# Kernel optimization log

Hardware: AMD Instinct MI355X
Metric: run time of the kernel (lower is better)

The kernel has to match this reference:

```python
import jax, jax.numpy as jnp
import numpy as np

K_SIZE = 5      # kernel_size
NUM_ITERS = 3   # num_iters
EPS = 1e-6


def _unfold(x, k):
    """Mimic F.unfold(x, k, padding=k//2) -> (B, N, K, D) with K=k*k, N=H*W.
    Channel ordering matches torch: unfold gives (B, D*K, N) with d-major, so
    view(B, D, K, N).permute(0, 3, 2, 1) == transpose below."""
    B, D, H, W = x.shape
    p = k // 2
    xp = jnp.pad(x, ((0, 0), (0, 0), (p, p), (p, p)))
    # stack k*k shifted views -> (B, D, K, H, W); loop is over the fixed 5x5 window
    patches = jnp.stack([xp[:, :, i:i + H, j:j + W]
                         for i in range(k) for j in range(k)], axis=2)
    return patches.reshape(B, D, k * k, H * W).transpose(0, 3, 2, 1)  # (B,N,K,D)


def setup_inputs() -> dict:
    key = jax.random.key(0)
    embeddings = jax.random.normal(key, (2, 32, 256, 256), dtype=jnp.float32)
    # init_bandwidth=1.0 -> log(exp(1)-1) so softplus(log_bandwidth)=1.0
    log_bandwidth = jnp.asarray(np.log(np.exp(1.0) - 1.0), dtype=jnp.float32)
    return {"embeddings": embeddings, "log_bandwidth": log_bandwidth}


def reference(embeddings, log_bandwidth):
    B, D, H, W = embeddings.shape
    N = H * W
    z = embeddings.reshape(B, D, N).transpose(0, 2, 1)  # (B, N, D)
    bandwidth = jax.nn.softplus(log_bandwidth)
    inv_2bw2 = 1.0 / (2.0 * bandwidth * bandwidth)
    # NOTE: original code unfolds `embeddings` (not z) every iter -> constant patches
    patches = _unfold(embeddings, K_SIZE)  # (B, N, K, D)
    for _ in range(NUM_ITERS):
        z_flat = jax.lax.stop_gradient(z)  # matches z.detach()
        diff = patches - z_flat[:, :, None, :]           # (B, N, K, D)
        dist2 = jnp.sum(diff * diff, axis=-1)            # (B, N, K)
        weights = jnp.exp(-dist2 * inv_2bw2)             # gaussian kernel
        numerator = jnp.einsum('bnk,bnkd->bnd', weights, patches)
        denom = jnp.sum(weights, axis=2, keepdims=True) + EPS
        z = numerator / denom
    # default flags: only shifted embeddings are returned
    return z.transpose(0, 2, 1).reshape(B, D, H, W)
```

## Files before the change

### kernel.cpp

```cpp
#include <hip/hip_runtime.h>
#include <math.h>


typedef _Float16 h2  __attribute__((ext_vector_type(2)));
typedef _Float16 h8  __attribute__((ext_vector_type(8)));
typedef unsigned int u4v __attribute__((ext_vector_type(4)));

constexpr int Dch  = 32;
constexpr int HH   = 256;
constexpr int WW   = 256;
constexpr int PADp = 2;
constexpr int BH   = 8;
constexpr int BW   = 16;
constexpr int TH   = BH + 2 * PADp;
constexpr int TWd  = BW + 2 * PADp;
constexpr int RSTR = 21;
constexpr int PSTR = TH * RSTR + 1;
constexpr int ITERS = 3;
constexpr int HWp  = HH * WW;
constexpr int NTHR = 512;

__device__ __forceinline__ float fdot2f(h2 a, h2 b, float c) {
    return __builtin_amdgcn_fdot2(a, b, c, false);
}

__device__ __forceinline__ float EXP2F(float x) {
#if __has_builtin(__builtin_amdgcn_exp2f)
    return __builtin_amdgcn_exp2f(x);
#else
    return __expf(x * 0.69314718055994531f);
#endif
}

__device__ __forceinline__ float qswap1(float x) {
    return __int_as_float(
        __builtin_amdgcn_mov_dpp(__float_as_int(x), 0xB1, 0xF, 0xF, true));
}
__device__ __forceinline__ float qswap2(float x) {
    return __int_as_float(
        __builtin_amdgcn_mov_dpp(__float_as_int(x), 0x4E, 0xF, 0xF, true));
}

__device__ __forceinline__ h2 as_h2(unsigned int x) {
    return __builtin_bit_cast(h2, x);
}

__global__ __launch_bounds__(NTHR, 4)
void meanshift_kernel(const float* __restrict__ E,
                      const float* __restrict__ lbw,
                      float* __restrict__ out)
{
    __shared__ u4v tile[4 * PSTR];

    const int bz  = blockIdx.z;
    const int oh  = blockIdx.y * BH - PADp;
    const int ow  = blockIdx.x * BW - PADp;
    const int tid = threadIdx.x;
    const int cq  = tid & 3;
    const int idx = tid >> 2;
    const int px  = idx & (BW - 1);
    const int py  = idx >> 4;

    const float bwv   = log1pf(__expf(lbw[0]));
    const float cc2   = 1.0f / (2.0f * bwv * bwv);
    const float negNC = -cc2 * 1.44269504f;

    const float* Eb = E + (size_t)bz * Dch * HWp;

    for (int job = tid; job < 4 * (TH * TWd); job += NTHR) {
        const int cc = job / (TH * TWd);
        const int p  = job - cc * (TH * TWd);
        const int tr = p / TWd;
        const int tc = p - tr * TWd;
        const int gh = oh + tr;
        const int gw = ow + tc;
        h8 v;
        if ((unsigned)gh < (unsigned)HH && (unsigned)gw < (unsigned)WW) {
            const float* p0 = Eb + (size_t)(8 * cc) * HWp + gh * WW + gw;
            #pragma unroll
            for (int k = 0; k < 8; ++k) v[k] = (_Float16)p0[k * HWp];
        } else {
            #pragma unroll
            for (int k = 0; k < 8; ++k) v[k] = (_Float16)0.f;
        }
        tile[cc * PSTR + tr * RSTR + tc] = __builtin_bit_cast(u4v, v);
    }
    __syncthreads();

    const u4v* __restrict__ tP = tile + cq * PSTR;

    const int rb0 = (py + 0) * RSTR + px;
    const int rb1 = (py + 1) * RSTR + px;
    const int rb2 = (py + 2) * RSTR + px;
    const int rb3 = (py + 3) * RSTR + px;
    const int rb4 = (py + 4) * RSTR + px;
    const u4v c00 = tP[rb0+0], c01 = tP[rb0+1], c02 = tP[rb0+2], c03 = tP[rb0+3], c04 = tP[rb0+4];
    const u4v c10 = tP[rb1+0], c11 = tP[rb1+1], c12 = tP[rb1+2], c13 = tP[rb1+3], c14 = tP[rb1+4];
    const u4v c20 = tP[rb2+0], c21 = tP[rb2+1], c22 = tP[rb2+2], c23 = tP[rb2+3], c24 = tP[rb2+4];
    const u4v c30 = tP[rb3+0], c31 = tP[rb3+1], c32 = tP[rb3+2], c33 = tP[rb3+3], c34 = tP[rb3+4];
    const u4v c40 = tP[rb4+0], c41 = tP[rb4+1], c42 = tP[rb4+2], c43 = tP[rb4+3], c44 = tP[rb4+4];

    h2 z0 = as_h2(c22[0]), z1 = as_h2(c22[1]);
    h2 z2 = as_h2(c22[2]), z3 = as_h2(c22[3]);

    float* Ob = out + (size_t)bz * Dch * HWp;
    const int off    = (oh + PADp + py) * WW + (ow + PADp + px);
    const int chbase = 8 * cq;

#define NBODY(Q) do {                                                         \
        const h2 p0 = as_h2(Q[0]), p1 = as_h2(Q[1]);                          \
        const h2 p2 = as_h2(Q[2]), p3 = as_h2(Q[3]);                          \
        const h2 e0 = p0 - z0, e1 = p1 - z1;                                  \
        const h2 e2 = p2 - z2, e3 = p3 - z3;                                  \
        float s0 = fdot2f(e0, e0, 0.f);                                       \
        float s1 = fdot2f(e1, e1, 0.f);                                       \
        s0 = fdot2f(e2, e2, s0);                                              \
        s1 = fdot2f(e3, e3, s1);                                              \
        const float dp = s0 + s1;                          \
        const float d2 = dp + qswap1(dp);                                     \
        const float dist = d2 + qswap2(d2);             \
        const float w = EXP2F(dist * negNC);                                  \
        den += w;                                                             \
        const _Float16 wh = (_Float16)w;                                      \
        const h2 w2v = {wh, wh};                                              \
        n0 += p0 * w2v; n1 += p1 * w2v;                                       \
        n2 += p2 * w2v; n3 += p3 * w2v;                                       \
    } while (0)

    #pragma unroll 1
    for (int it = 0; it < ITERS; ++it) {
        h2 n0 = {(_Float16)0.f, (_Float16)0.f};
        h2 n1 = n0, n2 = n0, n3 = n0;
        float den = 0.f;

        NBODY(c00); NBODY(c01); NBODY(c02); NBODY(c03); NBODY(c04);
        NBODY(c10); NBODY(c11); NBODY(c12); NBODY(c13); NBODY(c14);
        NBODY(c20); NBODY(c21); NBODY(c22); NBODY(c23); NBODY(c24);
        NBODY(c30); NBODY(c31); NBODY(c32); NBODY(c33); NBODY(c34);
        NBODY(c40); NBODY(c41); NBODY(c42); NBODY(c43); NBODY(c44);

        const float invf = 1.0f / (den + 1e-6f);
        if (it == ITERS - 1) {
#define WR(IDX, NV, EL) Ob[(size_t)(chbase + (IDX)) * HWp + off] = (float)NV[EL] * invf
            WR(0, n0, 0); WR(1, n0, 1); WR(2, n1, 0); WR(3, n1, 1);
            WR(4, n2, 0); WR(5, n2, 1); WR(6, n3, 0); WR(7, n3, 1);
#undef WR
        } else {
            const _Float16 ih = (_Float16)invf;
            const h2 iv = {ih, ih};
            z0 = n0 * iv; z1 = n1 * iv; z2 = n2 * iv; z3 = n3 * iv;
        }
    }
#undef NBODY
}

extern "C" void kernel_launch(void* const* d_in, const int* in_sizes, int n_in,
                              void* d_out, int out_size, void* d_ws, size_t ws_size,
                              hipStream_t stream) {
    const float* E   = (const float*)d_in[0];
    const float* lbw = (const float*)d_in[1];
    float* out       = (float*)d_out;

    const int B = in_sizes[0] / (Dch * HWp);
    dim3 grid(WW / BW, HH / BH, B);
    dim3 block(NTHR, 1, 1);
    hipLaunchKernelGGL(meanshift_kernel, grid, block, 0, stream, E, lbw, out);
}
```

Baseline: 38.85 us.

## Vectorize halo tile loads with float4 and prescale embeddings to fold bandwidth

Rewrites the shared-memory tile fill so each thread loads four adjacent pixels per channel with float4 global loads. This replaces scalar strided loads and the generic job loop, which should cut global load instructions. The tile is widened to 24 columns with a 4-aligned left edge. Embeddings are prescaled by sqrt(bandwidth constant) so the exp2 argument needs no multiply; the scale is undone at the final store. It also uses packed round-toward-zero fp16 conversions and lowers launch bounds occupancy from 4 to 2, which may affect register allocation and precision slightly.

After: 41.04 us. +5.6%, slower.

```diff
diff --git a/kernel.cpp b/kernel.cpp
--- a/kernel.cpp
+++ b/kernel.cpp
@@ -3,19 +3,17 @@
 
 
 typedef _Float16 h2  __attribute__((ext_vector_type(2)));
-typedef _Float16 h8  __attribute__((ext_vector_type(8)));
 typedef unsigned int u4v __attribute__((ext_vector_type(4)));
 
 constexpr int Dch  = 32;
 constexpr int HH   = 256;
 constexpr int WW   = 256;
-constexpr int PADp = 2;
 constexpr int BH   = 8;
 constexpr int BW   = 16;
-constexpr int TH   = BH + 2 * PADp;
-constexpr int TWd  = BW + 2 * PADp;
-constexpr int RSTR = 21;
-constexpr int PSTR = TH * RSTR + 1;
+constexpr int THs  = 12;
+constexpr int RSTR = 25;
+constexpr int PSTR = THs * RSTR + 1;
+constexpr int NJOB = 4 * THs * 6;
 constexpr int ITERS = 3;
 constexpr int HWp  = HH * WW;
 constexpr int NTHR = 512;
@@ -45,7 +43,19 @@
     return __builtin_bit_cast(h2, x);
 }
 
-__global__ __launch_bounds__(NTHR, 4)
+__device__ __forceinline__ h2 pk2(float a, float b) {
+#if __has_builtin(__builtin_amdgcn_cvt_pkrtz)
+    return __builtin_bit_cast(h2, __builtin_amdgcn_cvt_pkrtz(a, b));
+#else
+    h2 r; r[0] = (_Float16)a; r[1] = (_Float16)b; return r;
+#endif
+}
+
+__device__ __forceinline__ unsigned int pku(float a, float b) {
+    return __builtin_bit_cast(unsigned int, pk2(a, b));
+}
+
+__global__ __launch_bounds__(NTHR, 2)
 void meanshift_kernel(const float* __restrict__ E,
                       const float* __restrict__ lbw,
                       float* __restrict__ out)
@@ -53,47 +63,82 @@
     __shared__ u4v tile[4 * PSTR];
 
     const int bz  = blockIdx.z;
-    const int oh  = blockIdx.y * BH - PADp;
-    const int ow  = blockIdx.x * BW - PADp;
+    const int oh  = blockIdx.y * BH - 2;
+    const int owc = blockIdx.x * BW;
+    const int gw0 = owc - 4;
     const int tid = threadIdx.x;
     const int cq  = tid & 3;
     const int idx = tid >> 2;
     const int px  = idx & (BW - 1);
     const int py  = idx >> 4;
 
-    const float bwv   = log1pf(__expf(lbw[0]));
-    const float cc2   = 1.0f / (2.0f * bwv * bwv);
-    const float negNC = -cc2 * 1.44269504f;
+    const float bwv = log1pf(__expf(lbw[0]));
+    const float cc2 = 1.0f / (2.0f * bwv * bwv);
+    const float NCf = cc2 * 1.44269504f;
+    const float scl = __builtin_sqrtf(NCf);
+    const float isc = 1.0f / scl;
 
     const float* Eb = E + (size_t)bz * Dch * HWp;
 
-    for (int job = tid; job < 4 * (TH * TWd); job += NTHR) {
-        const int cc = job / (TH * TWd);
-        const int p  = job - cc * (TH * TWd);
-        const int tr = p / TWd;
-        const int tc = p - tr * TWd;
-        const int gh = oh + tr;
-        const int gw = ow + tc;
-        h8 v;
-        if ((unsigned)gh < (unsigned)HH && (unsigned)gw < (unsigned)WW) {
-            const float* p0 = Eb + (size_t)(8 * cc) * HWp + gh * WW + gw;
-            #pragma unroll
-            for (int k = 0; k < 8; ++k) v[k] = (_Float16)p0[k * HWp];
-        } else {
-            #pragma unroll
-            for (int k = 0; k < 8; ++k) v[k] = (_Float16)0.f;
+    if (tid < NJOB) {
+        const int cc  = tid / (THs * 6);
+        const int rem = tid - cc * (THs * 6);
+        const int row = rem / 6;
+        const int g   = rem - row * 6;
+        const int gh  = oh + row;
+        const int gwb = gw0 + 4 * g;
+
+        float4 F0 = {0.f,0.f,0.f,0.f}, F1 = F0, F2 = F0, F3 = F0;
+        float4 F4 = F0, F5 = F0, F6 = F0, F7 = F0;
+        if ((unsigned)gh < (unsigned)HH) {
+            const float* base = Eb + (size_t)(8 * cc) * HWp + gh * WW;
+            if (gwb >= 0 && gwb + 4 <= WW) {
+                F0 = *(const float4*)(base + 0 * (size_t)HWp + gwb);
+                F1 = *(const float4*)(base + 1 * (size_t)HWp + gwb);
+                F2 = *(const float4*)(base + 2 * (size_t)HWp + gwb);
+                F3 = *(const float4*)(base + 3 * (size_t)HWp + gwb);
+                F4 = *(const float4*)(base + 4 * (size_t)HWp + gwb);
+                F5 = *(const float4*)(base + 5 * (size_t)HWp + gwb);
+                F6 = *(const float4*)(base + 6 * (size_t)HWp + gwb);
+                F7 = *(const float4*)(base + 7 * (size_t)HWp + gwb);
+            } else {
+                const bool i0 = (unsigned)(gwb + 0) < (unsigned)WW;
+                const bool i1 = (unsigned)(gwb + 1) < (unsigned)WW;
+                const bool i2 = (unsigned)(gwb + 2) < (unsigned)WW;
+                const bool i3 = (unsigned)(gwb + 3) < (unsigned)WW;
+#define GE(K) F##K = make_float4( \
+                    i0 ? base[(K) * (size_t)HWp + gwb + 0] : 0.f, \
+                    i1 ? base[(K) * (size_t)HWp + gwb + 1] : 0.f, \
+                    i2 ? base[(K) * (size_t)HWp + gwb + 2] : 0.f, \
+                    i3 ? base[(K) * (size_t)HWp + gwb + 3] : 0.f)
+                GE(0); GE(1); GE(2); GE(3); GE(4); GE(5); GE(6); GE(7);
+#undef GE
+            }
         }
-        tile[cc * PSTR + tr * RSTR + tc] = __builtin_bit_cast(u4v, v);
+        const int wbase = cc * PSTR + row * RSTR + 4 * g;
+        u4v W;
+        W[0]=pku(F0.x*scl,F1.x*scl); W[1]=pku(F2.x*scl,F3.x*scl);
+        W[2]=pku(F4.x*scl,F5.x*scl); W[3]=pku(F6.x*scl,F7.x*scl);
+        tile[wbase + 0] = W;
+        W[0]=pku(F0.y*scl,F1.y*scl); W[1]=pku(F2.y*scl,F3.y*scl);
+        W[2]=pku(F4.y*scl,F5.y*scl); W[3]=pku(F6.y*scl,F7.y*scl);
+        tile[wbase + 1] = W;
+        W[0]=pku(F0.z*scl,F1.z*scl); W[1]=pku(F2.z*scl,F3.z*scl);
+        W[2]=pku(F4.z*scl,F5.z*scl); W[3]=pku(F6.z*scl,F7.z*scl);
+        tile[wbase + 2] = W;
+        W[0]=pku(F0.w*scl,F1.w*scl); W[1]=pku(F2.w*scl,F3.w*scl);
+        W[2]=pku(F4.w*scl,F5.w*scl); W[3]=pku(F6.w*scl,F7.w*scl);
+        tile[wbase + 3] = W;
     }
     __syncthreads();
 
     const u4v* __restrict__ tP = tile + cq * PSTR;
 
-    const int rb0 = (py + 0) * RSTR + px;
-    const int rb1 = (py + 1) * RSTR + px;
-    const int rb2 = (py + 2) * RSTR + px;
-    const int rb3 = (py + 3) * RSTR + px;
-    const int rb4 = (py + 4) * RSTR + px;
+    const int rb0 = (py + 0) * RSTR + (px + 2);
+    const int rb1 = rb0 + RSTR;
+    const int rb2 = rb1 + RSTR;
+    const int rb3 = rb2 + RSTR;
+    const int rb4 = rb3 + RSTR;
     const u4v c00 = tP[rb0+0], c01 = tP[rb0+1], c02 = tP[rb0+2], c03 = tP[rb0+3], c04 = tP[rb0+4];
     const u4v c10 = tP[rb1+0], c11 = tP[rb1+1], c12 = tP[rb1+2], c13 = tP[rb1+3], c14 = tP[rb1+4];
     const u4v c20 = tP[rb2+0], c21 = tP[rb2+1], c22 = tP[rb2+2], c23 = tP[rb2+3], c24 = tP[rb2+4];
@@ -104,7 +149,7 @@
     h2 z2 = as_h2(c22[2]), z3 = as_h2(c22[3]);
 
     float* Ob = out + (size_t)bz * Dch * HWp;
-    const int off    = (oh + PADp + py) * WW + (ow + PADp + px);
+    const int off    = (oh + 2 + py) * WW + (owc + px);
     const int chbase = 8 * cq;
 
 #define NBODY(Q) do {                                                         \
@@ -116,13 +161,12 @@
         float s1 = fdot2f(e1, e1, 0.f);                                       \
         s0 = fdot2f(e2, e2, s0);                                              \
         s1 = fdot2f(e3, e3, s1);                                              \
-        const float dp = s0 + s1;                          \
+        const float dp = s0 + s1;                       \
         const float d2 = dp + qswap1(dp);                                     \
-        const float dist = d2 + qswap2(d2);             \
-        const float w = EXP2F(dist * negNC);                                  \
+        const float d4 = d2 + qswap2(d2);                     \
+        const float w  = EXP2F(-d4);                \
         den += w;                                                             \
-        const _Float16 wh = (_Float16)w;                                      \
-        const h2 w2v = {wh, wh};                                              \
+        const h2 w2v = pk2(w, w);                                             \
         n0 += p0 * w2v; n1 += p1 * w2v;                                       \
         n2 += p2 * w2v; n3 += p3 * w2v;                                       \
     } while (0)
@@ -141,13 +185,13 @@
 
         const float invf = 1.0f / (den + 1e-6f);
         if (it == ITERS - 1) {
-#define WR(IDX, NV, EL) Ob[(size_t)(chbase + (IDX)) * HWp + off] = (float)NV[EL] * invf
+            const float fin = invf * isc;
+#define WR(IDX, NV, EL) Ob[(size_t)(chbase + (IDX)) * HWp + off] = (float)NV[EL] * fin
             WR(0, n0, 0); WR(1, n0, 1); WR(2, n1, 0); WR(3, n1, 1);
             WR(4, n2, 0); WR(5, n2, 1); WR(6, n3, 0); WR(7, n3, 1);
 #undef WR
         } else {
-            const _Float16 ih = (_Float16)invf;
-            const h2 iv = {ih, ih};
+            const h2 iv = pk2(invf, invf);
             z0 = n0 * iv; z1 = n1 * iv; z2 = n2 * iv; z3 = n3 * iv;
         }
     }
```
